# Optimization experiments

Measured on AMD Instinct MI355X. Metric: run time of the kernel, lower is better.

## Reference

```python
import jax, jax.numpy as jnp
import numpy as np

N = 8192
IN_DIM = 128
OUT_DIM = 128


def setup_inputs() -> dict:
    key = jax.random.key(0)
    k1, k2, k3, k4 = jax.random.split(key, 4)
    X = jax.random.normal(k1, (N, IN_DIM), dtype=jnp.float32)
    A = jax.random.uniform(k2, (N, N), dtype=jnp.float32)
    # Xavier-uniform linear weight [out, in], zero bias (as in reset_parameters)
    limit = float(np.sqrt(6.0 / (IN_DIM + OUT_DIM)))
    W = jax.random.uniform(k3, (OUT_DIM, IN_DIM), dtype=jnp.float32, minval=-limit, maxval=limit)
    b = jnp.zeros((OUT_DIM,), dtype=jnp.float32)
    return {"X": X, "A": A, "W": W, "b": b}


def reference(X, A, W, b):
    # A_hat = A + I  (add self-loops)
    A_hat = A + jnp.eye(A.shape[0], dtype=A.dtype)
    degree = A_hat.sum(axis=1)  # [N]
    d_inv_sqrt = degree ** -0.5
    d_inv_sqrt = jnp.where(jnp.isinf(d_inv_sqrt), 0.0, d_inv_sqrt)
    # D^{-1/2} A_hat D^{-1/2} as row/col scaling (same math as diag matmuls)
    A_norm = d_inv_sqrt[:, None] * A_hat * d_inv_sqrt[None, :]
    h = A_norm @ X  # [N, in_dim]
    return h @ W.T + b  # [N, out_dim]
```

## Files before the change

### kernel.cpp

```cpp
#include <hip/hip_runtime.h>
#include <hip/hip_bf16.h>

#define NN 8192
#define DIM 128
#define BM 16
#define BK 64
#define NT (NN / BK)

typedef __attribute__((ext_vector_type(4))) float f32x4;
typedef __attribute__((ext_vector_type(8))) short bf16x8;
typedef __attribute__((ext_vector_type(4))) short bf16x4;

static __device__ __forceinline__ short f2bf(float f) {
    __hip_bfloat16 h = __float2bfloat16(f);
    return *reinterpret_cast<short*>(&h);
}
static __device__ __forceinline__ float bf2f(short s) {
    union { unsigned int u; float f; } c;
    c.u = ((unsigned int)(unsigned short)s) << 16;
    return c.f;
}

static __device__ __forceinline__ void gload16(const void* g, void* l) {
    __builtin_amdgcn_global_load_lds(
        (const __attribute__((address_space(1))) unsigned int*)g,
        (__attribute__((address_space(3))) unsigned int*)l, 16, 0, 0);
}

__global__ __launch_bounds__(256) void k_rowsum(const float* __restrict__ A,
                                                float* __restrict__ dinv) {
    const int row = blockIdx.x;
    const int t = threadIdx.x;
    const float4* a4 = reinterpret_cast<const float4*>(A + (size_t)row * NN);
    float s = 0.f;
#pragma unroll
    for (int q = 0; q < 8; ++q) {
        float4 v = a4[q * 256 + t];
        s += (v.x + v.y) + (v.z + v.w);
    }
#pragma unroll
    for (int off = 32; off > 0; off >>= 1) s += __shfl_down(s, off);
    __shared__ float red[4];
    if ((t & 63) == 0) red[t >> 6] = s;
    __syncthreads();
    if (t == 0) {
        float deg = red[0] + red[1] + red[2] + red[3] + 1.0f;
        dinv[row] = 1.0f / sqrtf(deg);
    }
}

__global__ __launch_bounds__(256) void k_y(const float* __restrict__ X,
                                           const float* __restrict__ W,
                                           const float* __restrict__ dinv,
                                           short* __restrict__ Yt) {
    __shared__ float Wl[64 * 128];
    __shared__ float Xl[32 * 129];
    const int t = threadIdx.x;
    const int j0 = (blockIdx.x >> 1) * 32;
    const int half = blockIdx.x & 1;

    const float4* wg = reinterpret_cast<const float4*>(W + (size_t)half * 64 * 128);
#pragma unroll
    for (int q = 0; q < 8; ++q)
        reinterpret_cast<float4*>(Wl)[q * 256 + t] = wg[q * 256 + t];
#pragma unroll
    for (int q = 0; q < 4; ++q) {
        int p = q * 256 + t;
        int row = p >> 5, c4 = p & 31;
        float4 v = reinterpret_cast<const float4*>(X + (size_t)(j0 + row) * DIM)[c4];
        float* dst = Xl + row * 129 + c4 * 4;
        dst[0] = v.x; dst[1] = v.y; dst[2] = v.z; dst[3] = v.w;
    }
    __syncthreads();

    const int j = t & 31;
    const int fb = t >> 5;
    const float dj = dinv[j0 + j];
    float acc[8];
#pragma unroll
    for (int k = 0; k < 8; ++k) acc[k] = 0.f;
    for (int f = 0; f < DIM; ++f) {
        float xv = Xl[j * 129 + f];
#pragma unroll
        for (int k = 0; k < 8; ++k)
            acc[k] = fmaf(xv, Wl[(fb + k * 8) * 128 + f], acc[k]);
    }
#pragma unroll
    for (int k = 0; k < 8; ++k)
        Yt[(size_t)(half * 64 + fb + k * 8) * NN + j0 + j] = f2bf(dj * acc[k]);
}

__global__ __launch_bounds__(512, 4) void k_main(const float* __restrict__ A,
                                                 const short* __restrict__ Yt,
                                                 const float* __restrict__ dinv,
                                                 const float* __restrict__ bias,
                                                 float* __restrict__ out) {
    __shared__ short Ab[2][BM * BK];
    __shared__ short Yb[2][DIM * BK];

    const int t = threadIdx.x;
    const int i0 = blockIdx.x * BM;

    const int ar = t >> 4;
    const int ac4 = t & 15;
    const float4* aG = reinterpret_cast<const float4*>(A + (size_t)(i0 + (ar & 15)) * NN) + ac4;
    const int aLoff = ar * 128 + ((ac4 * 8) ^ ((ar & 7) << 4));

    const int yRow0 = t >> 3;
    const int ychunk = (t & 7) ^ (yRow0 & 7);
    const short* ySrc0 = Yt + (size_t)yRow0 * NN + ychunk * 8;
    const short* ySrc1 = Yt + (size_t)(yRow0 + 64) * NN + ychunk * 8;

    const int lane = t & 63;
    const int wid = t >> 6;
    const int l15 = lane & 15, lk = lane >> 4;
    const int f = wid * 16 + l15;
    const int swzA = (l15 & 7) << 4;
    int offA[2], offB[2];
#pragma unroll
    for (int kc = 0; kc < 2; ++kc) {
        const int bcol = kc * 64 + lk * 16;
        offA[kc] = l15 * 128 + (bcol ^ swzA);
        offB[kc] = f * 128 + (bcol ^ swzA);
    }

    f32x4 acc = {0.f, 0.f, 0.f, 0.f};

    gload16(ySrc0, (char*)Yb[0] + t * 16);
    gload16(ySrc1, (char*)Yb[0] + 8192 + t * 16);
    float4 avCur;
    if (t < 256) {
        float4 av0 = aG[0];
        bf16x4 a16 = { f2bf(av0.x), f2bf(av0.y), f2bf(av0.z), f2bf(av0.w) };
        *reinterpret_cast<bf16x4*>(reinterpret_cast<char*>(Ab[0]) + aLoff) = a16;
        avCur = aG[(NT > 1 ? 1 : 0) * 16];
    }
    __syncthreads();

    int cur = 0;
    for (int kt = 0; kt < NT; ++kt) {
        const int nxt  = (kt + 1 < NT) ? kt + 1 : NT - 1;
        const int nxt2 = (kt + 2 < NT) ? kt + 2 : NT - 1;

        char* ybw = reinterpret_cast<char*>(Yb[cur ^ 1]);
        gload16(ySrc0 + (size_t)nxt * BK, ybw + t * 16);
        gload16(ySrc1 + (size_t)nxt * BK, ybw + 8192 + t * 16);

        float4 avN;
        if (t < 256) avN = aG[nxt2 * 16];

        const char* ab = reinterpret_cast<const char*>(Ab[cur]);
        const char* yb = reinterpret_cast<const char*>(Yb[cur]);
        bf16x8 a0 = *reinterpret_cast<const bf16x8*>(ab + offA[0]);
        bf16x8 a1 = *reinterpret_cast<const bf16x8*>(ab + offA[1]);
        bf16x8 b0 = *reinterpret_cast<const bf16x8*>(yb + offB[0]);
        bf16x8 b1 = *reinterpret_cast<const bf16x8*>(yb + offB[1]);
        acc = __builtin_amdgcn_mfma_f32_16x16x32_bf16(a0, b0, acc, 0, 0, 0);
        acc = __builtin_amdgcn_mfma_f32_16x16x32_bf16(a1, b1, acc, 0, 0, 0);

        if (t < 256) {
            bf16x4 a16 = { f2bf(avCur.x), f2bf(avCur.y), f2bf(avCur.z), f2bf(avCur.w) };
            *reinterpret_cast<bf16x4*>(reinterpret_cast<char*>(Ab[cur ^ 1]) + aLoff) = a16;
            avCur = avN;
        }
        __syncthreads();
        cur ^= 1;
    }

    const int iBase = i0 + lk * 4;
    const float4 dv4 = *reinterpret_cast<const float4*>(dinv + iBase);
    const float dvr[4] = { dv4.x, dv4.y, dv4.z, dv4.w };
    const float bf_ = bias[f];
    bf16x4 yv = *reinterpret_cast<const bf16x4*>(Yt + (size_t)f * NN + iBase);
#pragma unroll
    for (int r = 0; r < 4; ++r) {
        float z = acc[r] + bf2f(yv[r]);
        out[(size_t)(iBase + r) * DIM + f] = dvr[r] * z + bf_;
    }
}

extern "C" void kernel_launch(void* const* d_in, const int* in_sizes, int n_in,
                              void* d_out, int out_size, void* d_ws, size_t ws_size,
                              hipStream_t stream) {
    (void)in_sizes; (void)n_in; (void)out_size; (void)ws_size;
    const float* X = (const float*)d_in[0];
    const float* A = (const float*)d_in[1];
    const float* W = (const float*)d_in[2];
    const float* b = (const float*)d_in[3];
    float* out = (float*)d_out;

    float* dinv = (float*)d_ws;
    short* Yt = (short*)((char*)d_ws + NN * sizeof(float));

    k_rowsum<<<NN, 256, 0, stream>>>(A, dinv);
    k_y<<<(NN / 32) * 2, 256, 0, stream>>>(X, W, dinv, Yt);
    k_main<<<NN / BM, 512, 0, stream>>>(A, Yt, dinv, b, out);
}
```

Measured before the change: 474.2 us.

## Load A and Y fragments straight from global into registers, dropping LDS staging

The main kernel no longer stages A and Yt tiles through double-buffered shared memory. Each lane now loads its own MFMA fragments directly from global memory, with one-step register prefetch, and converts A to bf16 in registers. The per-iteration block barrier becomes an occasional sync every eight tiles, kept only to hold waves roughly in step for cache reuse. This removes LDS traffic and barriers, but each of the 8 waves re-reads the same A rows from global/L2, and the per-lane access pattern is strided rather than coalesced.

Result: slower. 714.2 us (+50.6%).

```diff
diff --git a/kernel.cpp b/kernel.cpp
--- a/kernel.cpp
+++ b/kernel.cpp
@@ -20,11 +20,11 @@
     c.u = ((unsigned int)(unsigned short)s) << 16;
     return c.f;
 }
-
-static __device__ __forceinline__ void gload16(const void* g, void* l) {
-    __builtin_amdgcn_global_load_lds(
-        (const __attribute__((address_space(1))) unsigned int*)g,
-        (__attribute__((address_space(3))) unsigned int*)l, 16, 0, 0);
+static __device__ __forceinline__ bf16x8 cvt8(float4 a, float4 b) {
+    bf16x8 r;
+    r[0] = f2bf(a.x); r[1] = f2bf(a.y); r[2] = f2bf(a.z); r[3] = f2bf(a.w);
+    r[4] = f2bf(b.x); r[5] = f2bf(b.y); r[6] = f2bf(b.z); r[7] = f2bf(b.w);
+    return r;
 }
 
 __global__ __launch_bounds__(256) void k_rowsum(const float* __restrict__ A,
@@ -90,81 +90,48 @@
         Yt[(size_t)(half * 64 + fb + k * 8) * NN + j0 + j] = f2bf(dj * acc[k]);
 }
 
-__global__ __launch_bounds__(512, 4) void k_main(const float* __restrict__ A,
-                                                 const short* __restrict__ Yt,
-                                                 const float* __restrict__ dinv,
-                                                 const float* __restrict__ bias,
-                                                 float* __restrict__ out) {
-    __shared__ short Ab[2][BM * BK];
-    __shared__ short Yb[2][DIM * BK];
-
+__global__ __launch_bounds__(512) void k_main(const float* __restrict__ A,
+                                              const short* __restrict__ Yt,
+                                              const float* __restrict__ dinv,
+                                              const float* __restrict__ bias,
+                                              float* __restrict__ out) {
     const int t = threadIdx.x;
     const int i0 = blockIdx.x * BM;
-
-    const int ar = t >> 4;
-    const int ac4 = t & 15;
-    const float4* aG = reinterpret_cast<const float4*>(A + (size_t)(i0 + (ar & 15)) * NN) + ac4;
-    const int aLoff = ar * 128 + ((ac4 * 8) ^ ((ar & 7) << 4));
-
-    const int yRow0 = t >> 3;
-    const int ychunk = (t & 7) ^ (yRow0 & 7);
-    const short* ySrc0 = Yt + (size_t)yRow0 * NN + ychunk * 8;
-    const short* ySrc1 = Yt + (size_t)(yRow0 + 64) * NN + ychunk * 8;
-
     const int lane = t & 63;
     const int wid = t >> 6;
     const int l15 = lane & 15, lk = lane >> 4;
     const int f = wid * 16 + l15;
-    const int swzA = (l15 & 7) << 4;
-    int offA[2], offB[2];
-#pragma unroll
-    for (int kc = 0; kc < 2; ++kc) {
-        const int bcol = kc * 64 + lk * 16;
-        offA[kc] = l15 * 128 + (bcol ^ swzA);
-        offB[kc] = f * 128 + (bcol ^ swzA);
-    }
+
+    const float* aR = A + (size_t)(i0 + l15) * NN + lk * 8;
+    const short* yR = Yt + (size_t)f * NN + lk * 8;
 
     f32x4 acc = {0.f, 0.f, 0.f, 0.f};
 
-    gload16(ySrc0, (char*)Yb[0] + t * 16);
-    gload16(ySrc1, (char*)Yb[0] + 8192 + t * 16);
-    float4 avCur;
-    if (t < 256) {
-        float4 av0 = aG[0];
-        bf16x4 a16 = { f2bf(av0.x), f2bf(av0.y), f2bf(av0.z), f2bf(av0.w) };
-        *reinterpret_cast<bf16x4*>(reinterpret_cast<char*>(Ab[0]) + aLoff) = a16;
-        avCur = aG[(NT > 1 ? 1 : 0) * 16];
-    }
-    __syncthreads();
+    float4 a0l = *reinterpret_cast<const float4*>(aR);
+    float4 a0h = *reinterpret_cast<const float4*>(aR + 4);
+    float4 a1l = *reinterpret_cast<const float4*>(aR + 32);
+    float4 a1h = *reinterpret_cast<const float4*>(aR + 36);
+    bf16x8 y0 = *reinterpret_cast<const bf16x8*>(yR);
+    bf16x8 y1 = *reinterpret_cast<const bf16x8*>(yR + 32);
 
-    int cur = 0;
+#pragma unroll 2
     for (int kt = 0; kt < NT; ++kt) {
-        const int nxt  = (kt + 1 < NT) ? kt + 1 : NT - 1;
-        const int nxt2 = (kt + 2 < NT) ? kt + 2 : NT - 1;
+        const int nb = (kt + 1 < NT ? kt + 1 : kt) * BK;
 
-        char* ybw = reinterpret_cast<char*>(Yb[cur ^ 1]);
-        gload16(ySrc0 + (size_t)nxt * BK, ybw + t * 16);
-        gload16(ySrc1 + (size_t)nxt * BK, ybw + 8192 + t * 16);
+        float4 na0l = *reinterpret_cast<const float4*>(aR + nb);
+        float4 na0h = *reinterpret_cast<const float4*>(aR + nb + 4);
+        float4 na1l = *reinterpret_cast<const float4*>(aR + nb + 32);
+        float4 na1h = *reinterpret_cast<const float4*>(aR + nb + 36);
+        bf16x8 ny0 = *reinterpret_cast<const bf16x8*>(yR + nb);
+        bf16x8 ny1 = *reinterpret_cast<const bf16x8*>(yR + nb + 32);
 
-        float4 avN;
-        if (t < 256) avN = aG[nxt2 * 16];
+        acc = __builtin_amdgcn_mfma_f32_16x16x32_bf16(cvt8(a0l, a0h), y0, acc, 0, 0, 0);
+        acc = __builtin_amdgcn_mfma_f32_16x16x32_bf16(cvt8(a1l, a1h), y1, acc, 0, 0, 0);
 
-        const char* ab = reinterpret_cast<const char*>(Ab[cur]);
-        const char* yb = reinterpret_cast<const char*>(Yb[cur]);
-        bf16x8 a0 = *reinterpret_cast<const bf16x8*>(ab + offA[0]);
-        bf16x8 a1 = *reinterpret_cast<const bf16x8*>(ab + offA[1]);
-        bf16x8 b0 = *reinterpret_cast<const bf16x8*>(yb + offB[0]);
-        bf16x8 b1 = *reinterpret_cast<const bf16x8*>(yb + offB[1]);
-        acc = __builtin_amdgcn_mfma_f32_16x16x32_bf16(a0, b0, acc, 0, 0, 0);
-        acc = __builtin_amdgcn_mfma_f32_16x16x32_bf16(a1, b1, acc, 0, 0, 0);
+        a0l = na0l; a0h = na0h; a1l = na1l; a1h = na1h;
+        y0 = ny0; y1 = ny1;
 
-        if (t < 256) {
-            bf16x4 a16 = { f2bf(avCur.x), f2bf(avCur.y), f2bf(avCur.z), f2bf(avCur.w) };
-            *reinterpret_cast<bf16x4*>(reinterpret_cast<char*>(Ab[cur ^ 1]) + aLoff) = a16;
-            avCur = avN;
-        }
-        __syncthreads();
-        cur ^= 1;
+        if ((kt & 7) == 7) __syncthreads();
     }
 
     const int iBase = i0 + lk * 4;
```
